# Kernel optimization log

Measured on AMD Instinct MI355X. Metric: run time of the kernel, lower is better.

Reference implementation:

```python
import jax, jax.numpy as jnp
import numpy as np

B, S, D = 2, 2048, 1024
H = 16
HD = D // H  # 64
SCALE = HD ** -0.5


def setup_inputs() -> dict:
    key = jax.random.key(0)
    ks = jax.random.split(key, 9)
    init = lambda k, shape: jax.random.normal(k, shape, dtype=jnp.float32) * (1.0 / np.sqrt(shape[-1]))
    return {
        "x": jax.random.normal(ks[0], (B, S, D), dtype=jnp.float32),
        "wq": init(ks[1], (D, D)), "bq": jnp.zeros((D,), jnp.float32),
        "wk": init(ks[2], (D, D)), "bk": jnp.zeros((D,), jnp.float32),
        "wv": init(ks[3], (D, D)), "bv": jnp.zeros((D,), jnp.float32),
        "wo": init(ks[4], (D, D)), "bo": jnp.zeros((D,), jnp.float32),
    }


def reference(x, wq, bq, wk, bk, wv, bv, wo, bo):
    b, s, d = x.shape
    # projections -> [b, h, s, hd]
    q = (x @ wq + bq).reshape(b, s, H, HD).transpose(0, 2, 1, 3)
    k = (x @ wk + bk).reshape(b, s, H, HD).transpose(0, 2, 1, 3)
    v = (x @ wv + bv).reshape(b, s, H, HD).transpose(0, 2, 1, 3)
    # full causal attention (chunked loop in original computes exactly this)
    scores = jnp.einsum("bhqd,bhkd->bhqk", q, k) * SCALE
    causal = jnp.tril(jnp.ones((s, s), dtype=bool))
    scores = jnp.where(causal, scores, -jnp.inf)
    weights = jax.nn.softmax(scores, axis=-1)
    out = jnp.einsum("bhqk,bhkd->bhqd", weights, v)
    out = out.transpose(0, 2, 1, 3).reshape(b, s, d)
    return out @ wo + bo
```

## Files before the change

### kernel.cpp

```cpp
#include <hip/hip_runtime.h>
#include <hip/hip_bf16.h>
#include <cstdint>

#define B_  2
#define S_  2048
#define D_  1024
#define H_  16
#define HD_ 64
#define M_  (B_ * S_)
static constexpr float SC_LOG2E = 0.125f * 1.44269504088896f;

typedef __bf16 bf16x8 __attribute__((ext_vector_type(8)));
typedef __bf16 bf16x4 __attribute__((ext_vector_type(4)));
typedef float  f32x4  __attribute__((ext_vector_type(4)));

__device__ __forceinline__ unsigned short f2b(float f) {
  union { float f; unsigned u; } x; x.f = f;
  unsigned r = x.u + 0x7FFF + ((x.u >> 16) & 1);
  return (unsigned short)(r >> 16);
}

__device__ __forceinline__ void gl_lds16(const unsigned short* g, unsigned short* l) {
  __builtin_amdgcn_global_load_lds((const __attribute__((address_space(1))) void*)g,
                                   (__attribute__((address_space(3))) void*)l, 16, 0, 0);
}

__device__ __forceinline__ void bar_lgkm() {
  asm volatile("s_waitcnt lgkmcnt(0)\n\ts_barrier" ::: "memory");
}
__device__ __forceinline__ void bar_vm2() {
  asm volatile("s_waitcnt vmcnt(2) lgkmcnt(0)\n\ts_barrier" ::: "memory");
}
__device__ __forceinline__ void bar_vm0() {
  asm volatile("s_waitcnt vmcnt(0) lgkmcnt(0)\n\ts_barrier" ::: "memory");
}

__global__ void cvt_all_kernel(const float* __restrict__ x,
                               const float* __restrict__ w0, const float* __restrict__ w1,
                               const float* __restrict__ w2, const float* __restrict__ w3,
                               unsigned short* __restrict__ xb,
                               unsigned short* __restrict__ o0, unsigned short* __restrict__ o1,
                               unsigned short* __restrict__ o2, unsigned short* __restrict__ o3) {
  int tx = threadIdx.x, ty = threadIdx.y;
  if (blockIdx.z == 4) {
    int tid = ty * 32 + tx;
    int base = ((int)blockIdx.y * 32 + (int)blockIdx.x) * 1024 + tid;
    const float4* xf = (const float4*)x;
    ushort4* ob = (ushort4*)xb;
#pragma unroll
    for (int j = 0; j < 4; j++) {
      float4 v = xf[base + j * 256];
      ushort4 r;
      r.x = f2b(v.x); r.y = f2b(v.y); r.z = f2b(v.z); r.w = f2b(v.w);
      ob[base + j * 256] = r;
    }
    return;
  }
  const float* w = blockIdx.z == 0 ? w0 : blockIdx.z == 1 ? w1 : blockIdx.z == 2 ? w2 : w3;
  unsigned short* o = blockIdx.z == 0 ? o0 : blockIdx.z == 1 ? o1 : blockIdx.z == 2 ? o2 : o3;
  __shared__ float t[32][33];
  int x0 = blockIdx.x * 32, y0 = blockIdx.y * 32;
#pragma unroll
  for (int j = 0; j < 4; j++)
    t[ty + j * 8][tx] = w[(size_t)(y0 + ty + j * 8) * D_ + x0 + tx];
  __syncthreads();
#pragma unroll
  for (int j = 0; j < 4; j++)
    o[(size_t)(x0 + ty + j * 8) * D_ + y0 + tx] = f2b(t[tx][ty + j * 8]);
}

__global__ __launch_bounds__(512) void qkv_gemm_kernel(
    const unsigned short* __restrict__ xb,
    const unsigned short* __restrict__ wqt, const unsigned short* __restrict__ wkt,
    const unsigned short* __restrict__ wvt,
    const float* __restrict__ bq, const float* __restrict__ bk, const float* __restrict__ bv,
    unsigned short* __restrict__ qo, unsigned short* __restrict__ ko, unsigned short* __restrict__ vo) {
  const unsigned short* wt = blockIdx.z == 0 ? wqt : blockIdx.z == 1 ? wkt : wvt;
  const float* bias        = blockIdx.z == 0 ? bq  : blockIdx.z == 1 ? bk  : bv;
  unsigned short* out      = blockIdx.z == 0 ? qo  : blockIdx.z == 1 ? ko  : vo;
  const float scl = blockIdx.z == 0 ? SC_LOG2E : 1.0f;

  __shared__ __align__(16) unsigned short smem[6 * 4096];
  const int tid = threadIdx.x;
  const int lane = tid & 63, wid = tid >> 6;
  const int wm = wid & 1, wn = wid >> 1;
  const int m0 = blockIdx.x * 128, n0 = blockIdx.y * 128;
  const int l15 = lane & 15, q4 = lane >> 4;
  const int srow = tid >> 2, skc = (tid & 3) * 8;

  f32x4 zero = {0.f, 0.f, 0.f, 0.f};
  f32x4 acc[4][2];
#pragma unroll
  for (int mt = 0; mt < 4; mt++)
#pragma unroll
    for (int nt = 0; nt < 2; nt++) acc[mt][nt] = zero;

  const unsigned short* ap = xb + (size_t)(m0 + srow) * D_ + skc;
  const unsigned short* bp = wt + (size_t)(n0 + srow) * D_ + skc;
  gl_lds16(ap,      smem + tid * 8);
  gl_lds16(bp,      smem + 12288 + tid * 8);
  gl_lds16(ap + 32, smem + 4096 + tid * 8);
  gl_lds16(bp + 32, smem + 12288 + 4096 + tid * 8);

  int bc = 0;
  for (int it = 0; it < 32; it++) {
    if (it < 31) bar_vm2(); else bar_vm0();
    if (it + 2 < 32) {
      int bn_ = bc < 1 ? bc + 2 : bc - 1;
      gl_lds16(ap + (it + 2) * 32, smem + bn_ * 4096 + tid * 8);
      gl_lds16(bp + (it + 2) * 32, smem + 12288 + bn_ * 4096 + tid * 8);
    }
    const unsigned short* Ab = smem + bc * 4096;
    const unsigned short* Bb = smem + 12288 + bc * 4096;
    bf16x8 af[4], bfv[2];
#pragma unroll
    for (int mt = 0; mt < 4; mt++) af[mt]  = *(const bf16x8*)(Ab + (wm * 64 + mt * 16 + l15) * 32 + q4 * 8);
#pragma unroll
    for (int nt = 0; nt < 2; nt++) bfv[nt] = *(const bf16x8*)(Bb + (wn * 32 + nt * 16 + l15) * 32 + q4 * 8);
#pragma unroll
    for (int mt = 0; mt < 4; mt++)
#pragma unroll
      for (int nt = 0; nt < 2; nt++)
        acc[mt][nt] = __builtin_amdgcn_mfma_f32_16x16x32_bf16(af[mt], bfv[nt], acc[mt][nt], 0, 0, 0);
    bc = bc == 2 ? 0 : bc + 1;
  }

  if (blockIdx.z < 2) {
#pragma unroll
    for (int nt = 0; nt < 2; nt++) {
      int n = n0 + wn * 32 + nt * 16 + l15;
      float bn = bias[n];
      int h = n >> 6, hd = n & 63;
#pragma unroll
      for (int mt = 0; mt < 4; mt++) {
#pragma unroll
        for (int r = 0; r < 4; r++) {
          int m = m0 + wm * 64 + mt * 16 + q4 * 4 + r;
          int b = m >> 11, s = m & (S_ - 1);
          out[(((size_t)(b * H_ + h)) * S_ + s) * HD_ + hd] = f2b((acc[mt][nt][r] + bn) * scl);
        }
      }
    }
  } else {
    unsigned short* buf = smem;
#pragma unroll
    for (int p = 0; p < 2; p++) {
      __syncthreads();
      if ((wn >> 1) == p) {
#pragma unroll
        for (int nt = 0; nt < 2; nt++) {
          int np = (wn & 1) * 32 + nt * 16 + l15;
          float bn = bias[n0 + p * 64 + np];
#pragma unroll
          for (int mt = 0; mt < 4; mt++) {
            f32x4 vb = acc[mt][nt];
            vb[0] += bn; vb[1] += bn; vb[2] += bn; vb[3] += bn;
            bf16x4 pk = __builtin_convertvector(vb, bf16x4);
            *(bf16x4*)(&buf[np * 136 + wm * 64 + mt * 16 + q4 * 4]) = pk;
          }
        }
      }
      __syncthreads();
#pragma unroll
      for (int i = 0; i < 2; i++) {
        int ci = tid + i * 512;
        int np = ci >> 4, c = ci & 15;
        int n = n0 + p * 64 + np;
        int h = n >> 6, hd = n & 63;
        int m = m0 + c * 8;
        int b = m >> 11, s = m & (S_ - 1);
        *(uint4*)(out + (((size_t)(b * H_ + h)) * HD_ + hd) * S_ + s) = *(const uint4*)(buf + np * 136 + c * 8);
      }
    }
  }
}

__global__ __launch_bounds__(1024, 4) void attn_kernel(
    const unsigned short* __restrict__ Q, const unsigned short* __restrict__ K,
    const unsigned short* __restrict__ Vt_g, unsigned short* __restrict__ O) {
  const int id = blockIdx.x;
  const int bh = id & 31, x = id >> 5;
  const int b = bh >> 4, h = bh & 15;
  const unsigned short* Qh = Q    + (size_t)bh * S_ * HD_;
  const unsigned short* Kh = K    + (size_t)bh * S_ * HD_;
  const unsigned short* Vh = Vt_g + (size_t)bh * HD_ * S_;

  __shared__ __align__(16) unsigned short Ks[2][2][128 * 64];
  __shared__ __align__(16) unsigned short Vt[2][2][64 * 128];
  __shared__ __align__(16) unsigned short Ps[16][640];

  const int tid = threadIdx.x, lane = tid & 63, w = tid >> 6;
  const int hi = w >> 3, qw = w & 7;
  const int l15 = lane & 15, q4 = lane >> 4;
  const int st = tid >> 9, sid = tid & 511;
  const int krow0 = sid >> 3, kcol0 = (sid & 7) * 8;
  const int vrow0 = sid >> 4, vcol0 = (sid & 15) * 8;
  const int kc0s = kcol0 ^ ((krow0 & 7) << 3);
  const int vc0s = vcol0 ^ ((vrow0 & 7) << 3);
  const int kx = (l15 & 7) << 3;
  const int kcA = (q4 * 8) ^ kx, kcB = (q4 * 8 + 32) ^ kx;
  unsigned short* Pw = &Ps[w][0];
  const int pw0 = l15 * 40 + q4 * 4;
  const int pr0 = l15 * 40 + q4 * 8;
  float* scr = (float*)&Ks[0][0][0];
  float* sp = scr + (size_t)(qw * 64 + lane) * 20;

  f32x4 zero = {0.f, 0.f, 0.f, 0.f};
  int stc = 0;

  for (int hf = 0; hf < 2; hf++) {
    const int qi = hf ? 15 - x : x;
    const int q0 = qi * 128;
    const int nkt = qi + 1, nst = (nkt + 1) >> 1;

    const unsigned short* qp = Qh + (size_t)(q0 + qw * 16 + l15) * HD_ + q4 * 8;
    bf16x8 bq0 = *(const bf16x8*)(qp);
    bf16x8 bq1 = *(const bf16x8*)(qp + 32);
    const int qrow = q0 + qw * 16 + l15;

    float m_i = -1e30f, l_i = 0.f;
    f32x4 o_acc[4];
#pragma unroll
    for (int t4 = 0; t4 < 4; t4++) o_acc[t4] = zero;

    uint4 kp0 = {0,0,0,0}, kp1 = {0,0,0,0}, vp0 = {0,0,0,0}, vp1 = {0,0,0,0};
    if (st < nkt) {
      const int k0p = st * 128;
      kp0 = *(const uint4*)(Kh + (size_t)(k0p + krow0) * HD_ + kcol0);
      kp1 = *(const uint4*)(Kh + (size_t)(k0p + krow0 + 64) * HD_ + kcol0);
      vp0 = *(const uint4*)(Vh + (size_t)vrow0 * S_ + k0p + vcol0);
      vp1 = *(const uint4*)(Vh + (size_t)(vrow0 + 32) * S_ + k0p + vcol0);
    }

    for (int s = 0; s < nst; s++, stc++) {
      const int buf = stc & 1;
      {
        unsigned short* Kb = &Ks[buf][st][0];
        unsigned short* Vb = &Vt[buf][st][0];
        *(uint4*)(Kb + krow0 * 64 + kc0s) = kp0;
        *(uint4*)(Kb + (krow0 + 64) * 64 + kc0s) = kp1;
        *(uint4*)(Vb + vrow0 * 128 + vc0s) = vp0;
        *(uint4*)(Vb + (vrow0 + 32) * 128 + vc0s) = vp1;
      }
      bar_lgkm();
      const int ktn = 2 * (s + 1) + st;
      if (ktn < nkt) {
        const int k0n = ktn * 128;
        kp0 = *(const uint4*)(Kh + (size_t)(k0n + krow0) * HD_ + kcol0);
        kp1 = *(const uint4*)(Kh + (size_t)(k0n + krow0 + 64) * HD_ + kcol0);
        vp0 = *(const uint4*)(Vh + (size_t)vrow0 * S_ + k0n + vcol0);
        vp1 = *(const uint4*)(Vh + (size_t)(vrow0 + 32) * S_ + k0n + vcol0);
      }

      const int kt = 2 * s + hi;
      if (kt < nkt) {
        const int k0 = kt * 128;
        const unsigned short* Kb = &Ks[buf][hi][0];
        const unsigned short* Vb = &Vt[buf][hi][0];

        f32x4 sc[8];
#pragma unroll
        for (int nt = 0; nt < 8; nt++) sc[nt] = zero;
        __builtin_amdgcn_s_setprio(1);
#pragma unroll
        for (int nt = 0; nt < 8; nt++) {
          bf16x8 ak0 = *(const bf16x8*)(Kb + (nt * 16 + l15) * 64 + kcA);
          bf16x8 ak1 = *(const bf16x8*)(Kb + (nt * 16 + l15) * 64 + kcB);
          sc[nt] = __builtin_amdgcn_mfma_f32_16x16x32_bf16(ak0, bq0, sc[nt], 0, 0, 0);
          sc[nt] = __builtin_amdgcn_mfma_f32_16x16x32_bf16(ak1, bq1, sc[nt], 0, 0, 0);
        }
        __builtin_amdgcn_s_setprio(0);

        if ((k0 + 127) > (q0 + qw * 16)) {
#pragma unroll
          for (int nt = 0; nt < 8; nt++)
#pragma unroll
            for (int r = 0; r < 4; r++) {
              int key = k0 + nt * 16 + q4 * 4 + r;
              if (key > qrow) sc[nt][r] = -1e30f;
            }
        }

        float am[8];
#pragma unroll
        for (int nt = 0; nt < 8; nt++)
          am[nt] = fmaxf(fmaxf(sc[nt][0], sc[nt][1]), fmaxf(sc[nt][2], sc[nt][3]));
#pragma unroll
        for (int sr = 4; sr > 0; sr >>= 1)
#pragma unroll
          for (int i2 = 0; i2 < sr; i2++) am[i2] = fmaxf(am[i2], am[i2 + sr]);
        float mx = am[0];
        mx = fmaxf(mx, __shfl_xor(mx, 16));
        mx = fmaxf(mx, __shfl_xor(mx, 32));
        mx = fmaxf(mx, m_i);

        if (!__all(mx - m_i <= 10.0f)) {
          float alpha = __builtin_amdgcn_exp2f(m_i - mx);
          m_i = mx;
          l_i *= alpha;
#pragma unroll
          for (int r = 0; r < 4; r++) {
            float ar = __shfl(alpha, q4 * 4 + r);
            o_acc[0][r] *= ar; o_acc[1][r] *= ar; o_acc[2][r] *= ar; o_acc[3][r] *= ar;
          }
        }

        float sm[8];
#pragma unroll
        for (int nt = 0; nt < 8; nt++) {
          f32x4 pv;
#pragma unroll
          for (int r = 0; r < 4; r++) pv[r] = __builtin_amdgcn_exp2f(sc[nt][r] - m_i);
          sc[nt] = pv;
          sm[nt] = (pv[0] + pv[1]) + (pv[2] + pv[3]);
        }
#pragma unroll
        for (int sr = 4; sr > 0; sr >>= 1)
#pragma unroll
          for (int i2 = 0; i2 < sr; i2++) sm[i2] += sm[i2 + sr];
        float rs = sm[0];
        rs += __shfl_xor(rs, 16);
        rs += __shfl_xor(rs, 32);
        l_i += rs;

#pragma unroll
        for (int ks = 0; ks < 4; ks++) {
          bf16x4 pk0 = __builtin_convertvector(sc[2 * ks],     bf16x4);
          bf16x4 pk1 = __builtin_convertvector(sc[2 * ks + 1], bf16x4);
          *(bf16x4*)(Pw + pw0)      = pk0;
          *(bf16x4*)(Pw + pw0 + 16) = pk1;
          __threadfence_block();
          bf16x8 ap2 = *(const bf16x8*)(Pw + pr0);
          __builtin_amdgcn_s_setprio(1);
#pragma unroll
          for (int nt2 = 0; nt2 < 4; nt2++) {
            bf16x8 bv = *(const bf16x8*)(Vb + (nt2 * 16 + l15) * 128 + ((ks * 32 + q4 * 8) ^ kx));
            o_acc[nt2] = __builtin_amdgcn_mfma_f32_16x16x32_bf16(ap2, bv, o_acc[nt2], 0, 0, 0);
          }
          __builtin_amdgcn_s_setprio(0);
        }
      }
    }

    bar_lgkm();
    if (hi) {
      *(f32x4*)(sp + 0)  = o_acc[0];
      *(f32x4*)(sp + 4)  = o_acc[1];
      *(f32x4*)(sp + 8)  = o_acc[2];
      *(f32x4*)(sp + 12) = o_acc[3];
      sp[16] = m_i; sp[17] = l_i;
    }
    bar_lgkm();
    if (!hi) {
      f32x4 oh[4];
      oh[0] = *(const f32x4*)(sp + 0);
      oh[1] = *(const f32x4*)(sp + 4);
      oh[2] = *(const f32x4*)(sp + 8);
      oh[3] = *(const f32x4*)(sp + 12);
      float m_h = sp[16], l_h = sp[17];
      float M   = fmaxf(m_i, m_h);
      float a_l = __builtin_amdgcn_exp2f(m_i - M);
      float a_h = __builtin_amdgcn_exp2f(m_h - M);
      float l_f = l_i * a_l + l_h * a_h;
#pragma unroll
      for (int r = 0; r < 4; r++) {
        float arl = __shfl(a_l, q4 * 4 + r);
        float arh = __shfl(a_h, q4 * 4 + r);
        float inv = 1.0f / __shfl(l_f, q4 * 4 + r);
        int s_ = q0 + qw * 16 + q4 * 4 + r;
#pragma unroll
        for (int nt2 = 0; nt2 < 4; nt2++)
          O[((size_t)(b * S_ + s_)) * D_ + h * HD_ + nt2 * 16 + l15] =
              f2b((o_acc[nt2][r] * arl + oh[nt2][r] * arh) * inv);
      }
    }
    bar_lgkm();
  }
}

__global__ __launch_bounds__(512) void out_gemm_kernel(
    const unsigned short* __restrict__ ab, const unsigned short* __restrict__ wot,
    const float* __restrict__ bo, float* __restrict__ out) {
  __shared__ __align__(16) unsigned short smem[6 * 4096];
  const int tid = threadIdx.x;
  const int lane = tid & 63, wid = tid >> 6;
  const int wm = wid & 1, wn = wid >> 1;
  const int m0 = blockIdx.x * 128, n0 = blockIdx.y * 128;
  const int l15 = lane & 15, q4 = lane >> 4;
  const int srow = tid >> 2, skc = (tid & 3) * 8;

  f32x4 zero = {0.f, 0.f, 0.f, 0.f};
  f32x4 acc[4][2];
#pragma unroll
  for (int mt = 0; mt < 4; mt++)
#pragma unroll
    for (int nt = 0; nt < 2; nt++) acc[mt][nt] = zero;

  const unsigned short* ap = ab  + (size_t)(m0 + srow) * D_ + skc;
  const unsigned short* bp = wot + (size_t)(n0 + srow) * D_ + skc;
  gl_lds16(ap,      smem + tid * 8);
  gl_lds16(bp,      smem + 12288 + tid * 8);
  gl_lds16(ap + 32, smem + 4096 + tid * 8);
  gl_lds16(bp + 32, smem + 12288 + 4096 + tid * 8);

  int bc = 0;
  for (int it = 0; it < 32; it++) {
    if (it < 31) bar_vm2(); else bar_vm0();
    if (it + 2 < 32) {
      int bn_ = bc < 1 ? bc + 2 : bc - 1;
      gl_lds16(ap + (it + 2) * 32, smem + bn_ * 4096 + tid * 8);
      gl_lds16(bp + (it + 2) * 32, smem + 12288 + bn_ * 4096 + tid * 8);
    }
    const unsigned short* Ab = smem + bc * 4096;
    const unsigned short* Bb = smem + 12288 + bc * 4096;
    bf16x8 af[4], bfv[2];
#pragma unroll
    for (int mt = 0; mt < 4; mt++) af[mt]  = *(const bf16x8*)(Ab + (wm * 64 + mt * 16 + l15) * 32 + q4 * 8);
#pragma unroll
    for (int nt = 0; nt < 2; nt++) bfv[nt] = *(const bf16x8*)(Bb + (wn * 32 + nt * 16 + l15) * 32 + q4 * 8);
#pragma unroll
    for (int mt = 0; mt < 4; mt++)
#pragma unroll
      for (int nt = 0; nt < 2; nt++)
        acc[mt][nt] = __builtin_amdgcn_mfma_f32_16x16x32_bf16(af[mt], bfv[nt], acc[mt][nt], 0, 0, 0);
    bc = bc == 2 ? 0 : bc + 1;
  }

#pragma unroll
  for (int nt = 0; nt < 2; nt++) {
    int n = n0 + wn * 32 + nt * 16 + l15;
    float bn = bo[n];
#pragma unroll
    for (int mt = 0; mt < 4; mt++) {
#pragma unroll
      for (int r = 0; r < 4; r++) {
        int m = m0 + wm * 64 + mt * 16 + q4 * 4 + r;
        out[(size_t)m * D_ + n] = acc[mt][nt][r] + bn;
      }
    }
  }
}

extern "C" void kernel_launch(void* const* d_in, const int* in_sizes, int n_in,
                              void* d_out, int out_size, void* d_ws, size_t ws_size,
                              hipStream_t stream) {
  const float* x  = (const float*)d_in[0];
  const float* wq = (const float*)d_in[1];
  const float* bq = (const float*)d_in[2];
  const float* wk = (const float*)d_in[3];
  const float* bk = (const float*)d_in[4];
  const float* wv = (const float*)d_in[5];
  const float* bv = (const float*)d_in[6];
  const float* wo = (const float*)d_in[7];
  const float* bo = (const float*)d_in[8];
  float* out = (float*)d_out;

  char* ws = (char*)d_ws;
  unsigned short* xb  = (unsigned short*)(ws);
  unsigned short* wqt = (unsigned short*)(ws + (8u  << 20));
  unsigned short* wkt = (unsigned short*)(ws + (10u << 20));
  unsigned short* wvt = (unsigned short*)(ws + (12u << 20));
  unsigned short* wot = (unsigned short*)(ws + (14u << 20));
  unsigned short* qb  = (unsigned short*)(ws + (16u << 20));
  unsigned short* kb  = (unsigned short*)(ws + (24u << 20));
  unsigned short* vtg = (unsigned short*)(ws + (32u << 20));
  unsigned short* ab  = xb;

  cvt_all_kernel<<<dim3(32, 32, 5), dim3(32, 8), 0, stream>>>(x, wq, wk, wv, wo, xb, wqt, wkt, wvt, wot);
  qkv_gemm_kernel<<<dim3(32, 8, 3), dim3(512), 0, stream>>>(xb, wqt, wkt, wvt, bq, bk, bv, qb, kb, vtg);
  attn_kernel<<<dim3(256), dim3(1024), 0, stream>>>(qb, kb, vtg, ab);
  out_gemm_kernel<<<dim3(32, 8), dim3(512), 0, stream>>>(ab, wot, bo, out);
}
```

Measured before the change: 180.1 us.

## Halve attention block to 512 threads with two query groups per wave and async LDS loads

The attention kernel now runs 8 waves per block instead of 16, with each wave handling 32 query rows (two 16-row groups), so every K/V fragment read from LDS feeds twice as many MFMAs. K/V tiles are now loaded straight from global memory into LDS with global_load_lds and double-buffered, replacing the register-staged copy. The aim is to cut LDS read traffic per FLOP and shorten the load path. In exchange each wave holds more registers (two score and accumulator sets), and there are fewer waves to hide latency.

```diff
diff --git a/kernel.cpp b/kernel.cpp
--- a/kernel.cpp
+++ b/kernel.cpp
@@ -175,7 +175,7 @@
   }
 }
 
-__global__ __launch_bounds__(1024, 4) void attn_kernel(
+__global__ __launch_bounds__(512) void attn_kernel(
     const unsigned short* __restrict__ Q, const unsigned short* __restrict__ K,
     const unsigned short* __restrict__ Vt_g, unsigned short* __restrict__ O) {
   const int id = blockIdx.x;
@@ -187,23 +187,29 @@
 
   __shared__ __align__(16) unsigned short Ks[2][2][128 * 64];
   __shared__ __align__(16) unsigned short Vt[2][2][64 * 128];
-  __shared__ __align__(16) unsigned short Ps[16][640];
+  __shared__ __align__(16) unsigned short Ps[8][1280];
 
   const int tid = threadIdx.x, lane = tid & 63, w = tid >> 6;
-  const int hi = w >> 3, qw = w & 7;
+  const int hi = w >> 2, qw = w & 3;
   const int l15 = lane & 15, q4 = lane >> 4;
-  const int st = tid >> 9, sid = tid & 511;
-  const int krow0 = sid >> 3, kcol0 = (sid & 7) * 8;
-  const int vrow0 = sid >> 4, vcol0 = (sid & 15) * 8;
-  const int kc0s = kcol0 ^ ((krow0 & 7) << 3);
-  const int vc0s = vcol0 ^ ((vrow0 & 7) << 3);
   const int kx = (l15 & 7) << 3;
   const int kcA = (q4 * 8) ^ kx, kcB = (q4 * 8 + 32) ^ kx;
   unsigned short* Pw = &Ps[w][0];
-  const int pw0 = l15 * 40 + q4 * 4;
-  const int pr0 = l15 * 40 + q4 * 8;
   float* scr = (float*)&Ks[0][0][0];
-  float* sp = scr + (size_t)(qw * 64 + lane) * 20;
+  float* sp = scr + (size_t)(qw * 64 + lane) * 36;
+
+  const unsigned short* kg[2];
+  const unsigned short* vg[2];
+#pragma unroll
+  for (int j = 0; j < 2; j++) {
+    int li = tid + j * 512;
+    int krow = li >> 3;
+    int kcol = ((tid & 7) * 8) ^ ((krow & 7) * 8);
+    kg[j] = Kh + (size_t)krow * HD_ + kcol;
+    int vrow = li >> 4;
+    int vcol = ((tid & 15) * 8) ^ ((vrow & 7) * 8);
+    vg[j] = Vh + (size_t)vrow * S_ + vcol;
+  }
 
   f32x4 zero = {0.f, 0.f, 0.f, 0.f};
   int stc = 0;
@@ -213,129 +219,151 @@
     const int q0 = qi * 128;
     const int nkt = qi + 1, nst = (nkt + 1) >> 1;
 
-    const unsigned short* qp = Qh + (size_t)(q0 + qw * 16 + l15) * HD_ + q4 * 8;
-    bf16x8 bq0 = *(const bf16x8*)(qp);
-    bf16x8 bq1 = *(const bf16x8*)(qp + 32);
-    const int qrow = q0 + qw * 16 + l15;
-
-    float m_i = -1e30f, l_i = 0.f;
-    f32x4 o_acc[4];
-#pragma unroll
-    for (int t4 = 0; t4 < 4; t4++) o_acc[t4] = zero;
-
-    uint4 kp0 = {0,0,0,0}, kp1 = {0,0,0,0}, vp0 = {0,0,0,0}, vp1 = {0,0,0,0};
-    if (st < nkt) {
-      const int k0p = st * 128;
-      kp0 = *(const uint4*)(Kh + (size_t)(k0p + krow0) * HD_ + kcol0);
-      kp1 = *(const uint4*)(Kh + (size_t)(k0p + krow0 + 64) * HD_ + kcol0);
-      vp0 = *(const uint4*)(Vh + (size_t)vrow0 * S_ + k0p + vcol0);
-      vp1 = *(const uint4*)(Vh + (size_t)(vrow0 + 32) * S_ + k0p + vcol0);
+    bf16x8 bq[2][2];
+#pragma unroll
+    for (int g = 0; g < 2; g++) {
+      const unsigned short* qp = Qh + (size_t)(q0 + qw * 32 + g * 16 + l15) * HD_ + q4 * 8;
+      bq[g][0] = *(const bf16x8*)(qp);
+      bq[g][1] = *(const bf16x8*)(qp + 32);
+    }
+
+    float m_i[2] = {-1e30f, -1e30f}, l_i[2] = {0.f, 0.f};
+    f32x4 o_acc[2][4];
+#pragma unroll
+    for (int g = 0; g < 2; g++)
+#pragma unroll
+      for (int t4 = 0; t4 < 4; t4++) o_acc[g][t4] = zero;
+
+    {
+      const int bufn = stc & 1;
+#pragma unroll
+      for (int s2 = 0; s2 < 2; s2++) {
+        const int k0s = s2 * 128;
+        unsigned short* Kd = &Ks[bufn][s2][0];
+        unsigned short* Vd = &Vt[bufn][s2][0];
+#pragma unroll
+        for (int j = 0; j < 2; j++) {
+          gl_lds16(kg[j] + (size_t)k0s * HD_, Kd + (tid + j * 512) * 8);
+          gl_lds16(vg[j] + k0s,               Vd + (tid + j * 512) * 8);
+        }
+      }
     }
 
     for (int s = 0; s < nst; s++, stc++) {
-      const int buf = stc & 1;
-      {
-        unsigned short* Kb = &Ks[buf][st][0];
-        unsigned short* Vb = &Vt[buf][st][0];
-        *(uint4*)(Kb + krow0 * 64 + kc0s) = kp0;
-        *(uint4*)(Kb + (krow0 + 64) * 64 + kc0s) = kp1;
-        *(uint4*)(Vb + vrow0 * 128 + vc0s) = vp0;
-        *(uint4*)(Vb + (vrow0 + 32) * 128 + vc0s) = vp1;
-      }
-      bar_lgkm();
-      const int ktn = 2 * (s + 1) + st;
-      if (ktn < nkt) {
-        const int k0n = ktn * 128;
-        kp0 = *(const uint4*)(Kh + (size_t)(k0n + krow0) * HD_ + kcol0);
-        kp1 = *(const uint4*)(Kh + (size_t)(k0n + krow0 + 64) * HD_ + kcol0);
-        vp0 = *(const uint4*)(Vh + (size_t)vrow0 * S_ + k0n + vcol0);
-        vp1 = *(const uint4*)(Vh + (size_t)(vrow0 + 32) * S_ + k0n + vcol0);
+      const int bufc = stc & 1;
+      bar_vm0();
+      if (s + 1 < nst) {
+        const int bufn = bufc ^ 1;
+#pragma unroll
+        for (int s2 = 0; s2 < 2; s2++) {
+          const int k0s = (2 * (s + 1) + s2) * 128;
+          unsigned short* Kd = &Ks[bufn][s2][0];
+          unsigned short* Vd = &Vt[bufn][s2][0];
+#pragma unroll
+          for (int j = 0; j < 2; j++) {
+            gl_lds16(kg[j] + (size_t)k0s * HD_, Kd + (tid + j * 512) * 8);
+            gl_lds16(vg[j] + k0s,               Vd + (tid + j * 512) * 8);
+          }
+        }
       }
 
       const int kt = 2 * s + hi;
       if (kt < nkt) {
         const int k0 = kt * 128;
-        const unsigned short* Kb = &Ks[buf][hi][0];
-        const unsigned short* Vb = &Vt[buf][hi][0];
-
-        f32x4 sc[8];
-#pragma unroll
-        for (int nt = 0; nt < 8; nt++) sc[nt] = zero;
+        const unsigned short* Kb = &Ks[bufc][hi][0];
+        const unsigned short* Vb = &Vt[bufc][hi][0];
+
+        f32x4 sc[2][8];
+#pragma unroll
+        for (int g = 0; g < 2; g++)
+#pragma unroll
+          for (int nt = 0; nt < 8; nt++) sc[g][nt] = zero;
         __builtin_amdgcn_s_setprio(1);
 #pragma unroll
         for (int nt = 0; nt < 8; nt++) {
           bf16x8 ak0 = *(const bf16x8*)(Kb + (nt * 16 + l15) * 64 + kcA);
           bf16x8 ak1 = *(const bf16x8*)(Kb + (nt * 16 + l15) * 64 + kcB);
-          sc[nt] = __builtin_amdgcn_mfma_f32_16x16x32_bf16(ak0, bq0, sc[nt], 0, 0, 0);
-          sc[nt] = __builtin_amdgcn_mfma_f32_16x16x32_bf16(ak1, bq1, sc[nt], 0, 0, 0);
+          sc[0][nt] = __builtin_amdgcn_mfma_f32_16x16x32_bf16(ak0, bq[0][0], sc[0][nt], 0, 0, 0);
+          sc[0][nt] = __builtin_amdgcn_mfma_f32_16x16x32_bf16(ak1, bq[0][1], sc[0][nt], 0, 0, 0);
+          sc[1][nt] = __builtin_amdgcn_mfma_f32_16x16x32_bf16(ak0, bq[1][0], sc[1][nt], 0, 0, 0);
+          sc[1][nt] = __builtin_amdgcn_mfma_f32_16x16x32_bf16(ak1, bq[1][1], sc[1][nt], 0, 0, 0);
         }
         __builtin_amdgcn_s_setprio(0);
 
-        if ((k0 + 127) > (q0 + qw * 16)) {
+#pragma unroll
+        for (int g = 0; g < 2; g++) {
+          const int qrow = q0 + qw * 32 + g * 16 + l15;
+          if ((k0 + 127) > (q0 + qw * 32 + g * 16)) {
+#pragma unroll
+            for (int nt = 0; nt < 8; nt++)
+#pragma unroll
+              for (int r = 0; r < 4; r++) {
+                int key = k0 + nt * 16 + q4 * 4 + r;
+                if (key > qrow) sc[g][nt][r] = -1e30f;
+              }
+          }
+          float am[8];
 #pragma unroll
           for (int nt = 0; nt < 8; nt++)
+            am[nt] = fmaxf(fmaxf(sc[g][nt][0], sc[g][nt][1]), fmaxf(sc[g][nt][2], sc[g][nt][3]));
+#pragma unroll
+          for (int sr = 4; sr > 0; sr >>= 1)
+#pragma unroll
+            for (int i2 = 0; i2 < sr; i2++) am[i2] = fmaxf(am[i2], am[i2 + sr]);
+          float mx = am[0];
+          mx = fmaxf(mx, __shfl_xor(mx, 16));
+          mx = fmaxf(mx, __shfl_xor(mx, 32));
+          mx = fmaxf(mx, m_i[g]);
+
+          if (!__all(mx - m_i[g] <= 10.0f)) {
+            float alpha = __builtin_amdgcn_exp2f(m_i[g] - mx);
+            m_i[g] = mx;
+            l_i[g] *= alpha;
 #pragma unroll
             for (int r = 0; r < 4; r++) {
-              int key = k0 + nt * 16 + q4 * 4 + r;
-              if (key > qrow) sc[nt][r] = -1e30f;
+              float ar = __shfl(alpha, q4 * 4 + r);
+              o_acc[g][0][r] *= ar; o_acc[g][1][r] *= ar;
+              o_acc[g][2][r] *= ar; o_acc[g][3][r] *= ar;
             }
-        }
-
-        float am[8];
-#pragma unroll
-        for (int nt = 0; nt < 8; nt++)
-          am[nt] = fmaxf(fmaxf(sc[nt][0], sc[nt][1]), fmaxf(sc[nt][2], sc[nt][3]));
-#pragma unroll
-        for (int sr = 4; sr > 0; sr >>= 1)
-#pragma unroll
-          for (int i2 = 0; i2 < sr; i2++) am[i2] = fmaxf(am[i2], am[i2 + sr]);
-        float mx = am[0];
-        mx = fmaxf(mx, __shfl_xor(mx, 16));
-        mx = fmaxf(mx, __shfl_xor(mx, 32));
-        mx = fmaxf(mx, m_i);
-
-        if (!__all(mx - m_i <= 10.0f)) {
-          float alpha = __builtin_amdgcn_exp2f(m_i - mx);
-          m_i = mx;
-          l_i *= alpha;
-#pragma unroll
-          for (int r = 0; r < 4; r++) {
-            float ar = __shfl(alpha, q4 * 4 + r);
-            o_acc[0][r] *= ar; o_acc[1][r] *= ar; o_acc[2][r] *= ar; o_acc[3][r] *= ar;
-          }
-        }
-
-        float sm[8];
-#pragma unroll
-        for (int nt = 0; nt < 8; nt++) {
-          f32x4 pv;
-#pragma unroll
-          for (int r = 0; r < 4; r++) pv[r] = __builtin_amdgcn_exp2f(sc[nt][r] - m_i);
-          sc[nt] = pv;
-          sm[nt] = (pv[0] + pv[1]) + (pv[2] + pv[3]);
-        }
-#pragma unroll
-        for (int sr = 4; sr > 0; sr >>= 1)
-#pragma unroll
-          for (int i2 = 0; i2 < sr; i2++) sm[i2] += sm[i2 + sr];
-        float rs = sm[0];
-        rs += __shfl_xor(rs, 16);
-        rs += __shfl_xor(rs, 32);
-        l_i += rs;
+          }
+
+          float sm[8];
+#pragma unroll
+          for (int nt = 0; nt < 8; nt++) {
+            f32x4 pv;
+#pragma unroll
+            for (int r = 0; r < 4; r++) pv[r] = __builtin_amdgcn_exp2f(sc[g][nt][r] - m_i[g]);
+            sc[g][nt] = pv;
+            sm[nt] = (pv[0] + pv[1]) + (pv[2] + pv[3]);
+          }
+#pragma unroll
+          for (int sr = 4; sr > 0; sr >>= 1)
+#pragma unroll
+            for (int i2 = 0; i2 < sr; i2++) sm[i2] += sm[i2 + sr];
+          float rs = sm[0];
+          rs += __shfl_xor(rs, 16);
+          rs += __shfl_xor(rs, 32);
+          l_i[g] += rs;
+        }
 
 #pragma unroll
         for (int ks = 0; ks < 4; ks++) {
-          bf16x4 pk0 = __builtin_convertvector(sc[2 * ks],     bf16x4);
-          bf16x4 pk1 = __builtin_convertvector(sc[2 * ks + 1], bf16x4);
-          *(bf16x4*)(Pw + pw0)      = pk0;
-          *(bf16x4*)(Pw + pw0 + 16) = pk1;
+#pragma unroll
+          for (int g = 0; g < 2; g++) {
+            bf16x4 pk0 = __builtin_convertvector(sc[g][2 * ks],     bf16x4);
+            bf16x4 pk1 = __builtin_convertvector(sc[g][2 * ks + 1], bf16x4);
+            *(bf16x4*)(Pw + (g * 16 + l15) * 40 + q4 * 4)      = pk0;
+            *(bf16x4*)(Pw + (g * 16 + l15) * 40 + 16 + q4 * 4) = pk1;
+          }
           __threadfence_block();
-          bf16x8 ap2 = *(const bf16x8*)(Pw + pr0);
+          bf16x8 ap0 = *(const bf16x8*)(Pw + l15 * 40 + q4 * 8);
+          bf16x8 ap1 = *(const bf16x8*)(Pw + (16 + l15) * 40 + q4 * 8);
           __builtin_amdgcn_s_setprio(1);
 #pragma unroll
           for (int nt2 = 0; nt2 < 4; nt2++) {
             bf16x8 bv = *(const bf16x8*)(Vb + (nt2 * 16 + l15) * 128 + ((ks * 32 + q4 * 8) ^ kx));
-            o_acc[nt2] = __builtin_amdgcn_mfma_f32_16x16x32_bf16(ap2, bv, o_acc[nt2], 0, 0, 0);
+            o_acc[0][nt2] = __builtin_amdgcn_mfma_f32_16x16x32_bf16(ap0, bv, o_acc[0][nt2], 0, 0, 0);
+            o_acc[1][nt2] = __builtin_amdgcn_mfma_f32_16x16x32_bf16(ap1, bv, o_acc[1][nt2], 0, 0, 0);
           }
           __builtin_amdgcn_s_setprio(0);
         }
@@ -344,34 +372,36 @@
 
     bar_lgkm();
     if (hi) {
-      *(f32x4*)(sp + 0)  = o_acc[0];
-      *(f32x4*)(sp + 4)  = o_acc[1];
-      *(f32x4*)(sp + 8)  = o_acc[2];
-      *(f32x4*)(sp + 12) = o_acc[3];
-      sp[16] = m_i; sp[17] = l_i;
+#pragma unroll
+      for (int g = 0; g < 2; g++)
+#pragma unroll
+        for (int t4 = 0; t4 < 4; t4++) *(f32x4*)(sp + g * 16 + t4 * 4) = o_acc[g][t4];
+      sp[32] = m_i[0]; sp[33] = m_i[1];
+      sp[34] = l_i[0]; sp[35] = l_i[1];
     }
     bar_lgkm();
     if (!hi) {
-      f32x4 oh[4];
-      oh[0] = *(const f32x4*)(sp + 0);
-      oh[1] = *(const f32x4*)(sp + 4);
-      oh[2] = *(const f32x4*)(sp + 8);
-      oh[3] = *(const f32x4*)(sp + 12);
-      float m_h = sp[16], l_h = sp[17];
-      float M   = fmaxf(m_i, m_h);
-      float a_l = __builtin_amdgcn_exp2f(m_i - M);
-      float a_h = __builtin_amdgcn_exp2f(m_h - M);
-      float l_f = l_i * a_l + l_h * a_h;
-#pragma unroll
-      for (int r = 0; r < 4; r++) {
-        float arl = __shfl(a_l, q4 * 4 + r);
-        float arh = __shfl(a_h, q4 * 4 + r);
-        float inv = 1.0f / __shfl(l_f, q4 * 4 + r);
-        int s_ = q0 + qw * 16 + q4 * 4 + r;
-#pragma unroll
-        for (int nt2 = 0; nt2 < 4; nt2++)
-          O[((size_t)(b * S_ + s_)) * D_ + h * HD_ + nt2 * 16 + l15] =
-              f2b((o_acc[nt2][r] * arl + oh[nt2][r] * arh) * inv);
+#pragma unroll
+      for (int g = 0; g < 2; g++) {
+        f32x4 oh[4];
+#pragma unroll
+        for (int t4 = 0; t4 < 4; t4++) oh[t4] = *(const f32x4*)(sp + g * 16 + t4 * 4);
+        float m_h = sp[32 + g], l_h = sp[34 + g];
+        float M   = fmaxf(m_i[g], m_h);
+        float a_l = __builtin_amdgcn_exp2f(m_i[g] - M);
+        float a_h = __builtin_amdgcn_exp2f(m_h - M);
+        float l_f = l_i[g] * a_l + l_h * a_h;
+#pragma unroll
+        for (int r = 0; r < 4; r++) {
+          float arl = __shfl(a_l, q4 * 4 + r);
+          float arh = __shfl(a_h, q4 * 4 + r);
+          float inv = 1.0f / __shfl(l_f, q4 * 4 + r);
+          int s_ = q0 + qw * 32 + g * 16 + q4 * 4 + r;
+#pragma unroll
+          for (int nt2 = 0; nt2 < 4; nt2++)
+            O[((size_t)(b * S_ + s_)) * D_ + h * HD_ + nt2 * 16 + l15] =
+                f2b((o_acc[g][nt2][r] * arl + oh[nt2][r] * arh) * inv);
+        }
       }
     }
     bar_lgkm();
@@ -468,6 +498,6 @@
 
   cvt_all_kernel<<<dim3(32, 32, 5), dim3(32, 8), 0, stream>>>(x, wq, wk, wv, wo, xb, wqt, wkt, wvt, wot);
   qkv_gemm_kernel<<<dim3(32, 8, 3), dim3(512), 0, stream>>>(xb, wqt, wkt, wvt, bq, bk, bv, qb, kb, vtg);
-  attn_kernel<<<dim3(256), dim3(1024), 0, stream>>>(qb, kb, vtg, ab);
+  attn_kernel<<<dim3(256), dim3(512), 0, stream>>>(qb, kb, vtg, ab);
   out_gemm_kernel<<<dim3(32, 8), dim3(512), 0, stream>>>(ab, wot, bo, out);
 }
```

Result: no change. 177.1 us (-1.7%).
